# Kernel tuning notes

Measured on AMD Instinct MI355X. Metric: run time of the kernel, lower is better.

Reference implementation:

```python
import jax, jax.numpy as jnp
import numpy as np

K = 3        # kernel_size
EPS = 1e-4   # eps from __init__


def _conv_valid(x, w):
    # NHWC input, HWIO filter, VALID padding, stride 1
    return jax.lax.conv_general_dilated(
        x, w, window_strides=(1, 1), padding='VALID',
        dimension_numbers=('NHWC', 'HWIO', 'NHWC'))


def _backward_standardize_weight(grad_in, original_weights, gain, w_max_bitmap, eps):
    # Faithful translation of BackwardInjectWSConv2D.backward_standardize_weight
    kh, kw, cin, cout = original_weights.shape
    N = float(kh * kw * cin)                       # b*h*w in the TF code
    mu = jnp.mean(original_weights, axis=(0, 1, 2))
    xmu = original_weights - mu                    # [K,K,Cin,Cout]
    var = jnp.mean(jnp.square(xmu), axis=(0, 1, 2))
    mvar = N * var
    maxvar = jnp.maximum(mvar, eps)
    sqrtvar = jnp.sqrt(maxvar)
    ivar = 1.0 / sqrtvar
    givar = gain * ivar                            # [Cout]
    dgivar = jnp.sum(grad_in * xmu, axis=(0, 1, 2))
    divar = dgivar * gain
    dgain = dgivar * ivar
    dxmu1 = grad_in * givar
    dsqrtvar = (-1.0 / jnp.square(sqrtvar)) * divar
    dmaxvar = (0.5 / jnp.sqrt(maxvar)) * dsqrtvar
    dmvar = w_max_bitmap * dmaxvar
    dvar = N * dmvar
    dsq = (1.0 / N) * dvar                         # (1/N)*ones_like(grad_in)*dvar, broadcast
    dxmu2 = 2.0 * xmu * dsq
    dx1 = dxmu1 + dxmu2
    dmu = -jnp.sum(dx1, axis=(0, 1, 2))
    dx2 = (1.0 / N) * dmu                          # broadcast over [K,K,Cin]
    dx = dx1 + dx2
    return dx, dgain


def setup_inputs() -> dict:
    key = jax.random.key(0)
    ks = jax.random.split(key, 5)
    B, H, W, Cin, Cout = 64, 56, 56, 128, 128
    return {
        'grad_output': jax.random.normal(ks[0], (B, H, W, Cout), jnp.float32),
        'inputs': jax.random.normal(ks[1], (B, H, W, Cin), jnp.float32),
        'kernels': jax.random.normal(ks[2], (K, K, Cin, Cout), jnp.float32),
        'std_kernels': jax.random.normal(ks[3], (K, K, Cin, Cout), jnp.float32),
        'gain': jax.random.uniform(ks[4], (Cout,), jnp.float32),
        'w_max_bitmap': jnp.ones((Cout,), jnp.float32),
    }


def reference(grad_output, inputs, kernels, std_kernels, gain, w_max_bitmap):
    pad = (K - 1) // 2
    # ---- grad wrt input: full conv of grad_out with rot180(std_kernels), io swapped
    go_pad = jnp.pad(grad_output, ((0, 0), (pad, pad), (pad, pad), (0, 0)))
    w_rot = jnp.transpose(std_kernels[::-1, ::-1], (0, 1, 3, 2))   # [K,K,Cout,Cin]
    manual_grad_in = _conv_valid(go_pad, w_rot)                    # [B,H,W,Cin]
    # ---- grad wrt weight: treat Cin as batch, B as contraction channel
    in_pad = jnp.pad(inputs, ((0, 0), (pad, pad), (pad, pad), (0, 0)))
    fmt_inp = jnp.transpose(in_pad, (3, 1, 2, 0))                  # [Cin,H+2p,W+2p,B]
    fmt_wt = jnp.transpose(grad_output, (1, 2, 0, 3))              # [H,W,B,Cout]
    direct = _conv_valid(fmt_inp, fmt_wt)                          # [Cin,K,K,Cout]
    grad_wt_raw = jnp.transpose(direct, (1, 2, 0, 3))              # [K,K,Cin,Cout]
    # ---- weight-standardization backward chain
    manual_grad_wt, manual_grad_gain = _backward_standardize_weight(
        grad_wt_raw, kernels, gain, w_max_bitmap, EPS)
    # ---- bias grad
    manual_grad_bias = jnp.sum(grad_output, axis=(0, 1, 2))        # [Cout]
    return manual_grad_in, manual_grad_wt, manual_grad_bias, manual_grad_gain
```

## Files before the change

### kernel.cpp

```cpp
#include <hip/hip_runtime.h>
#include <hip/hip_bf16.h>

typedef __bf16 bf16x8 __attribute__((ext_vector_type(8)));
typedef __bf16 bf16x4 __attribute__((ext_vector_type(4)));
typedef float  f32x4  __attribute__((ext_vector_type(4)));
typedef unsigned int u32;

#define HW_   3136
#define NPIX  200704
#define GI_ELEMS 25690112

#define GOT_OFF   0u
#define RAW_OFF   51380224u
#define BIASA_OFF 51970048u
#define STDKF_OFF 51970560u
#define GUARD_OFF 52265472u
#define ZB_OFF    52265728u
#define ZA_OFF    52272000u
#define X_OFF     52279168u

__device__ __forceinline__ f32x4 mfma16(bf16x8 a, bf16x8 b, f32x4 c){
  return __builtin_amdgcn_mfma_f32_16x16x32_bf16(a, b, c, 0, 0, 0);
}

__device__ __forceinline__ void async16(const void* g, __bf16* l){
  __builtin_amdgcn_global_load_lds(
      (const __attribute__((address_space(1))) void*)g,
      (__attribute__((address_space(3))) void*)l, 16, 0, 0);
}

__global__ __launch_bounds__(256) void k_prep(const float* __restrict__ s, __bf16* __restrict__ d){
  const int g = blockIdx.x*256 + threadIdx.x;
  const int l = g & 63;
  const int j = (g >> 6) & 7;
  const int kc = (g >> 9) & 3;
  const int tap = g >> 11;
  const int ci = j*16 + (l & 15);
  const int co0 = kc*32 + (l >> 4)*8;
  const float* src = s + ((size_t)(tap*128 + ci))*128 + co0;
  f32x4 x0 = *(const f32x4*)src;
  f32x4 x1 = *(const f32x4*)(src + 4);
  bf16x8 y;
  #pragma unroll
  for (int e=0;e<4;e++){ y[e] = (__bf16)x0[e]; y[e+4] = (__bf16)x1[e]; }
  *(bf16x8*)(d + (size_t)g*8) = y;
}

__global__ __launch_bounds__(256) void k_goT(const float* __restrict__ go,
                                             __bf16* __restrict__ goT,
                                             __bf16* __restrict__ goB,
                                             float* __restrict__ biasA){
  __shared__ __bf16 T[64][130];
  __shared__ float biasS[128];
  const int t = threadIdx.x;
  const size_t p0 = (size_t)blockIdx.x*64;
  if (t < 128) biasS[t] = 0.f;
  __syncthreads();
  float bs[4] = {0.f,0.f,0.f,0.f};
  const int co0 = (t*4) & 127;
  #pragma unroll
  for (int i=0;i<8;i++){
    const int flat = (i*256+t)*4;
    const int px = flat >> 7, co = flat & 127;
    f32x4 x = *(const f32x4*)(go + p0*128 + flat);
    bf16x4 y;
    #pragma unroll
    for (int e=0;e<4;e++){ y[e] = (__bf16)x[e]; bs[e] += x[e]; }
    *(bf16x4*)&T[px][co] = y;
    *(bf16x4*)(goB + p0*128 + flat) = y;
  }
  #pragma unroll
  for (int e=0;e<4;e++) atomicAdd(&biasS[co0+e], bs[e]);
  __syncthreads();
  #pragma unroll
  for (int j=0;j<2;j++){
    const int task = j*256 + t;
    const int co = task >> 2, q = task & 3;
    bf16x8 v0, v1;
    #pragma unroll
    for (int k=0;k<8;k++) v0[k] = T[q*16+k][co];
    #pragma unroll
    for (int k=0;k<8;k++) v1[k] = T[q*16+8+k][co];
    __bf16* d = goT + (size_t)co*NPIX + p0 + q*16;
    *(bf16x8*)d = v0; *(bf16x8*)(d+8) = v1;
  }
  if (t < 128) atomicAdd(&biasA[t], biasS[t]);
}

__global__ __launch_bounds__(256) void k_inT(const float* __restrict__ inp,
                                             __bf16* __restrict__ inT){
  __shared__ __bf16 T[64][130];
  const int t = threadIdx.x;
  const size_t p0 = (size_t)blockIdx.x*64;

  if (blockIdx.x < 2304){
    const int g = blockIdx.x*256 + t;
    const int pair = g / 72, k = g - pair*72;
    __bf16* base = inT + (size_t)pair*3712;
    int off;
    if (k < 8)       off = k*8;
    else if (k < 16) off = 57*64 + (k-8)*8;
    else             off = (k-15)*64 + 56;
    bf16x8 z = {};
    *(bf16x8*)(base + off) = z;
  }

  #pragma unroll
  for (int i=0;i<8;i++){
    const int flat = (i*256+t)*4;
    const int px = flat >> 7, ci = flat & 127;
    f32x4 x = *(const f32x4*)(inp + p0*128 + flat);
    bf16x4 y;
    #pragma unroll
    for (int e=0;e<4;e++) y[e] = (__bf16)x[e];
    *(bf16x4*)&T[px][ci] = y;
  }
  __syncthreads();
  #pragma unroll
  for (int j=0;j<4;j++){
    const int task = j*256 + t;
    const int ci = task >> 3, ch = task & 7;
    const int p = (int)p0 + ch*8;
    const int b = p / HW_; const int r = p - b*HW_;
    const int h = r / 56;  const int w = r - h*56;
    bf16x8 v;
    #pragma unroll
    for (int k=0;k<8;k++) v[k] = T[ch*8+k][ci];
    *(bf16x8*)(inT + (((size_t)(ci*64+b))*58 + (h+1))*64 + w) = v;
  }
}

__global__ __launch_bounds__(512, 2) void k_gradin5(const __bf16* __restrict__ goB,
                                                    const __bf16* __restrict__ stdkF,
                                                    const __bf16* __restrict__ zsrc,
                                                    float* __restrict__ out){
  __shared__ char LDS[74240];
  const int t = threadIdx.x;
  const int wv = t >> 6, l = t & 63, lr = l & 15, lg = l >> 4;
  const int b = blockIdx.x, h0 = blockIdx.y*8;
  const int j0 = (wv & 1)*4;
  const int pxg = (wv >> 1)*112;

  int sb[7];
  #pragma unroll
  for (int tile=0; tile<7; ++tile){
    const int p = pxg + tile*16 + lr;
    const int ro = p / 56; const int w = p - ro*56;
    sb[tile] = (ro + 2)*58 + (w + 2);
  }

  f32x4 acc[7][4];
  #pragma unroll
  for (int i=0;i<7;i++){
    #pragma unroll
    for (int j=0;j<4;j++){
      #pragma unroll
      for (int r=0;r<4;r++) acc[i][j][r] = 0.f;
    }
  }

  for (int c=0; c<2; ++c){
    #pragma unroll
    for (int it=0; it<10; ++it){
      const int qb = it*512 + wv*64;
      const u32 q = (u32)(qb + l);
      if (q < 4640u){
        const u32 r = q / 464u;
        const u32 rem = q - r*464u;
        const u32 wp = rem >> 3;
        const u32 cl = rem & 7u;
        const int h = h0 - 1 + (int)r;
        const u32 s = r*58u + wp;
        const u32 csrc = cl ^ (s & 7u);
        const bool valid = (h >= 0) & (h < 56) & (wp >= 1u) & (wp <= 56u);
        const __bf16* src = valid
          ? goB + ((size_t)((b*HW_) + h*56 + ((int)wp - 1))*128 + c*64 + csrc*8)
          : zsrc;
        async16(src, (__bf16*)(LDS + qb*16));
      }
    }
    __syncthreads();

    for (int tap=0; tap<9; ++tap){
      const int u = tap/3;
      const int soff = u*58 + (tap - u*3);
      #pragma unroll
      for (int kc=0; kc<2; ++kc){
        const int kcg = c*2 + kc;
        bf16x8 Bf[4];
        #pragma unroll
        for (int j=0;j<4;++j)
          Bf[j] = *(const bf16x8*)(stdkF + ((size_t)(((tap*4 + kcg)*8 + j0 + j)*64 + l))*8);
        bf16x8 Af[7];
        #pragma unroll
        for (int tile=0;tile<7;++tile){
          const int s = sb[tile] - soff;
          const int byte = (s << 7) | (((kc*4 + lg) ^ (s & 7)) << 4);
          Af[tile] = *(const bf16x8*)(LDS + byte);
        }
        #pragma unroll
        for (int tile=0;tile<7;++tile){
          #pragma unroll
          for (int j=0;j<4;++j)
            acc[tile][j] = mfma16(Af[tile], Bf[j], acc[tile][j]);
        }
      }
    }
    __syncthreads();
  }

  float* o = out + ((size_t)b*HW_ + (size_t)h0*56 + pxg)*128;
  #pragma unroll
  for (int tile=0;tile<7;++tile){
    #pragma unroll
    for (int j=0;j<4;++j){
      #pragma unroll
      for (int r=0;r<4;++r)
        o[(size_t)(tile*16 + 4*lg + r)*128 + (j0 + j)*16 + lr] = acc[tile][j][r];
    }
  }
}

#define KSTEP9(ks)                                                             \
{                                                                              \
  const int pl = (ks)*32 + lg*8;                                               \
  const int q  = (ks)*4 + lg;                                                  \
  const int hl = q / 7;                                                        \
  const int w0 = pl - hl*56;                                                   \
  const int plc = ((ks)==3 && lg==3) ? 112 : pl;                               \
  bf16x8 b0 = *(const bf16x8*)&Bb[(wco + lr)*120 + plc];                       \
  bf16x8 b1 = *(const bf16x8*)&Bb[(wco + 16 + lr)*120 + plc];                  \
  const __bf16* abase = &Ab[lr*264 + hl*64 + w0];                              \
  _Pragma("unroll")                                                            \
  for (int u=0; u<3; ++u){                                                     \
    const __bf16* ap = abase + u*64;                                           \
    union { bf16x8 v; u32 d[4]; } vp, va, vn, a0, a2;                          \
    vp.v = *(const bf16x8*)(ap - 8);                                           \
    va.v = *(const bf16x8*)ap;                                                 \
    vn.v = *(const bf16x8*)(ap + 8);                                           \
    if ((ks)==3 && lg >= 2){                                                   \
      vp.d[0]=0u; vp.d[1]=0u; vp.d[2]=0u; vp.d[3]=0u;                          \
      va.d[0]=0u; va.d[1]=0u; va.d[2]=0u; va.d[3]=0u;                          \
      vn.d[0]=0u; vn.d[1]=0u; vn.d[2]=0u; vn.d[3]=0u;                          \
    }                                                                          \
    a0.d[0] = (va.d[0] << 16) | (vp.d[3] >> 16);                               \
    a0.d[1] = (va.d[1] << 16) | (va.d[0] >> 16);                               \
    a0.d[2] = (va.d[2] << 16) | (va.d[1] >> 16);                               \
    a0.d[3] = (va.d[3] << 16) | (va.d[2] >> 16);                               \
    a2.d[0] = (va.d[0] >> 16) | (va.d[1] << 16);                               \
    a2.d[1] = (va.d[1] >> 16) | (va.d[2] << 16);                               \
    a2.d[2] = (va.d[2] >> 16) | (va.d[3] << 16);                               \
    a2.d[3] = (va.d[3] >> 16) | (vn.d[0] << 16);                               \
    acc[u*3+0][0] = mfma16(a0.v, b0, acc[u*3+0][0]);                           \
    acc[u*3+0][1] = mfma16(a0.v, b1, acc[u*3+0][1]);                           \
    acc[u*3+1][0] = mfma16(va.v, b0, acc[u*3+1][0]);                           \
    acc[u*3+1][1] = mfma16(va.v, b1, acc[u*3+1][1]);                           \
    acc[u*3+2][0] = mfma16(a2.v, b0, acc[u*3+2][0]);                           \
    acc[u*3+2][1] = mfma16(a2.v, b1, acc[u*3+2][1]);                           \
  }                                                                            \
}

__global__ __launch_bounds__(256, 2) void k_gradwt9(const char* __restrict__ ws,
                                                    float* __restrict__ raw){
  __shared__ __bf16 LDS[39208];
  const int t = threadIdx.x;
  const int w = t >> 6, l = t & 63, lr = l & 15, lg = l >> 4;
  const int b = blockIdx.x, ci0 = blockIdx.y*16;
  const int wco = w*32;

  if (t < 40){
    const int idx = (t < 8) ? (30720 + t) : ((t < 24) ? (34952 + t - 8) : (39192 + t - 24));
    LDS[idx] = (__bf16)0.f;
  }

  u32 boff[8];
  #pragma unroll
  for (int i=0;i<8;i++){
    const int chunk = i*256 + t;
    if (chunk < 1920){
      const int co = chunk / 15, part = chunk - co*15;
      boff[i] = (part < 14)
        ? (GOT_OFF + (u32)(co*NPIX + b*HW_ + part*8)*2u)
        : ZB_OFF;
    } else boff[i] = ZB_OFF;
  }
  u32 aoff[3];
  #pragma unroll
  for (int i=0;i<3;i++){
    const int chunk = i*256 + t;
    if (chunk < 528){
      const int ci = chunk / 33, r = chunk - ci*33;
      aoff[i] = (r < 32)
        ? (X_OFF + (u32)((((ci0+ci)*64 + b)*58 + (r>>3))*64 + (r&7)*8)*2u)
        : ZA_OFF;
    } else aoff[i] = ZA_OFF;
  }

  f32x4 acc[9][2];
  #pragma unroll
  for (int tp=0;tp<9;tp++){
    #pragma unroll
    for (int j=0;j<2;j++){
      #pragma unroll
      for (int r=0;r<4;r++) acc[tp][j][r] = 0.f;
    }
  }

  #pragma unroll
  for (int i=0;i<8;i++){
    const int chunk = i*256 + t;
    if (chunk < 1920){ async16(ws + boff[i], LDS + chunk*8); boff[i] += 224u; }
  }
  #pragma unroll
  for (int i=0;i<3;i++){
    const int chunk = i*256 + t;
    if (chunk < 528){ async16(ws + aoff[i], LDS + 30728 + chunk*8); aoff[i] += 256u; }
  }
  __syncthreads();

  for (int c=0; c<28; ++c){
    const int cur = c & 1;
    if (c < 27){
      __bf16* dB = LDS + ((cur ^ 1) ? 15360 : 0);
      __bf16* dA = LDS + ((cur ^ 1) ? 34968 : 30728);
      #pragma unroll
      for (int i=0;i<8;i++){
        const int chunk = i*256 + t;
        if (chunk < 1920){ async16(ws + boff[i], dB + chunk*8); boff[i] += 224u; }
      }
      #pragma unroll
      for (int i=0;i<3;i++){
        const int chunk = i*256 + t;
        if (chunk < 528){ async16(ws + aoff[i], dA + chunk*8); aoff[i] += 256u; }
      }
    }
    const __bf16* Bb = LDS + (cur ? 15360 : 0);
    const __bf16* Ab = LDS + (cur ? 34968 : 30728);
    KSTEP9(0) KSTEP9(1) KSTEP9(2) KSTEP9(3)
    __syncthreads();
  }

  #pragma unroll
  for (int tp=0;tp<9;tp++){
    #pragma unroll
    for (int j=0;j<2;j++){
      #pragma unroll
      for (int r=0;r<4;r++)
        atomicAdd(&raw[(size_t)(tp*128 + ci0 + 4*lg + r)*128 + wco + j*16 + lr],
                  acc[tp][j][r]);
    }
  }
}

__global__ __launch_bounds__(128) void k_std(const float* __restrict__ raw,
      const float* __restrict__ kern, const float* __restrict__ gain,
      const float* __restrict__ bmap, const float* __restrict__ biasA,
      float* __restrict__ out_wt, float* __restrict__ out_bias, float* __restrict__ out_gain){
  const int co = blockIdx.x, t = threadIdx.x;
  float kv[9], gv[9];
  float s1=0.f, s2=0.f, sg=0.f, sgk=0.f;
  #pragma unroll
  for (int i=0;i<9;i++){
    const int m = t + i*128;
    const float k_ = kern[(size_t)m*128 + co];
    const float g_ = raw [(size_t)m*128 + co];
    kv[i]=k_; gv[i]=g_;
    s1 += k_; s2 += k_*k_; sg += g_; sgk += g_*k_;
  }
  __shared__ float red[4][128];
  red[0][t]=s1; red[1][t]=s2; red[2][t]=sg; red[3][t]=sgk;
  __syncthreads();
  for (int off=64; off>0; off>>=1){
    if (t < off){
      red[0][t]+=red[0][t+off]; red[1][t]+=red[1][t+off];
      red[2][t]+=red[2][t+off]; red[3][t]+=red[3][t+off];
    }
    __syncthreads();
  }
  const float N = 1152.f;
  const float S1=red[0][0], S2=red[1][0], Sg=red[2][0], Sgk=red[3][0];
  const float mu = S1/N;
  const float var = S2/N - mu*mu;
  const float mvar = N*var;
  const float maxvar = fmaxf(mvar, 1e-4f);
  const float sqrtvar = sqrtf(maxvar);
  const float ivar = 1.f/sqrtvar;
  const float g = gain[co];
  const float givar = g*ivar;
  const float dgivar = Sgk - mu*Sg;
  const float divar = dgivar*g;
  const float dsqrtvar = -divar/maxvar;
  const float dmaxvar = 0.5f*dsqrtvar/sqrtvar;
  const float dsq = bmap[co]*dmaxvar;
  const float dmu = -(givar*Sg + 2.f*dsq*(S1 - N*mu));
  const float dmuN = dmu*(1.f/N);
  #pragma unroll
  for (int i=0;i<9;i++){
    const int m = t + i*128;
    out_wt[(size_t)m*128 + co] = gv[i]*givar + 2.f*(kv[i]-mu)*dsq + dmuN;
  }
  if (t == 0){ out_gain[co] = dgivar*ivar; out_bias[co] = biasA[co]; }
}

extern "C" void kernel_launch(void* const* d_in, const int* in_sizes, int n_in,
                              void* d_out, int out_size, void* d_ws, size_t ws_size,
                              hipStream_t stream){
  const float* go   = (const float*)d_in[0];
  const float* inp  = (const float*)d_in[1];
  const float* kern = (const float*)d_in[2];
  const float* stdk = (const float*)d_in[3];
  const float* gain = (const float*)d_in[4];
  const float* bmap = (const float*)d_in[5];

  char* ws = (char*)d_ws;
  __bf16* goT   = (__bf16*)(ws + GOT_OFF);
  float*  raw   = (float*) (ws + RAW_OFF);
  float*  biasA = (float*) (ws + BIASA_OFF);
  __bf16* stdkF = (__bf16*)(ws + STDKF_OFF);
  char*   guard =           ws + GUARD_OFF;
  __bf16* goB   = (__bf16*)(ws + X_OFF);
  __bf16* inT   = (__bf16*)(ws + X_OFF);

  hipMemsetAsync(ws + RAW_OFF,   0, 589824 + 512, stream);
  hipMemsetAsync(ws + GUARD_OFF, 0, 256 + 6272 + 7168, stream);

  k_prep  <<<72, 256, 0, stream>>>(stdk, stdkF);
  k_goT   <<<3136, 256, 0, stream>>>(go, goT, goB, biasA);
  k_gradin5<<<dim3(64,7), 512, 0, stream>>>(goB, stdkF, (const __bf16*)guard, (float*)d_out);

  k_inT   <<<3136, 256, 0, stream>>>(inp, inT);
  k_gradwt9<<<dim3(64,8), 256, 0, stream>>>((const char*)ws, raw);

  float* out = (float*)d_out;
  k_std<<<128, 128, 0, stream>>>(raw, kern, gain, bmap, biasA,
                                 out + GI_ELEMS,
                                 out + GI_ELEMS + 147456,
                                 out + GI_ELEMS + 147456 + 128);
}
```

Before: 300.5 us.

## Split weight-gradient kernel over image halves and drop double buffering for occupancy

The weight-gradient kernel now splits each image's rows into two halves via a third grid dimension, which doubles the block count and adds more atomic accumulation into the raw buffer. The double-buffered LDS pipeline is replaced by a single buffer with load, sync, compute, sync. This halves shared memory per block so the launch bound can allow four blocks per CU instead of two. The aim is to hide memory latency through occupancy and more parallel blocks rather than software prefetch, at the cost of exposed load latency within each block and twice the atomics.

```diff
diff --git a/kernel.cpp b/kernel.cpp
--- a/kernel.cpp
+++ b/kernel.cpp
@@ -221,16 +221,20 @@
   }
 }
 
-#define KSTEP9(ks)                                                             \
+#define GWX_G0 15360
+#define GWX_A  15368
+#define GWX_G1 19592
+
+#define KSTEP10(ks)                                                            \
 {                                                                              \
   const int pl = (ks)*32 + lg*8;                                               \
   const int q  = (ks)*4 + lg;                                                  \
   const int hl = q / 7;                                                        \
   const int w0 = pl - hl*56;                                                   \
   const int plc = ((ks)==3 && lg==3) ? 112 : pl;                               \
-  bf16x8 b0 = *(const bf16x8*)&Bb[(wco + lr)*120 + plc];                       \
-  bf16x8 b1 = *(const bf16x8*)&Bb[(wco + 16 + lr)*120 + plc];                  \
-  const __bf16* abase = &Ab[lr*264 + hl*64 + w0];                              \
+  bf16x8 b0 = *(const bf16x8*)&LDS[(wco + lr)*120 + plc];                      \
+  bf16x8 b1 = *(const bf16x8*)&LDS[(wco + 16 + lr)*120 + plc];                 \
+  const __bf16* abase = &LDS[GWX_A + lr*264 + hl*64 + w0];                     \
   _Pragma("unroll")                                                            \
   for (int u=0; u<3; ++u){                                                     \
     const __bf16* ap = abase + u*64;                                           \
@@ -260,19 +264,20 @@
   }                                                                            \
 }
 
-__global__ __launch_bounds__(256, 2) void k_gradwt9(const char* __restrict__ ws,
-                                                    float* __restrict__ raw){
-  __shared__ __bf16 LDS[39208];
+__global__ __launch_bounds__(256, 4) void k_gradwt10(const char* __restrict__ ws,
+                                                     float* __restrict__ raw){
+  __shared__ __bf16 LDS[19608];
   const int t = threadIdx.x;
   const int w = t >> 6, l = t & 63, lr = l & 15, lg = l >> 4;
-  const int b = blockIdx.x, ci0 = blockIdx.y*16;
+  const int b = blockIdx.x, ci0 = blockIdx.y*16, hh = blockIdx.z;
   const int wco = w*32;
 
-  if (t < 40){
-    const int idx = (t < 8) ? (30720 + t) : ((t < 24) ? (34952 + t - 8) : (39192 + t - 24));
+  if (t < 24){
+    const int idx = (t < 8) ? (GWX_G0 + t) : (GWX_G1 + t - 8);
     LDS[idx] = (__bf16)0.f;
   }
 
+  const int pixbase = b*HW_ + hh*1568;
   u32 boff[8];
   #pragma unroll
   for (int i=0;i<8;i++){
@@ -280,7 +285,7 @@
     if (chunk < 1920){
       const int co = chunk / 15, part = chunk - co*15;
       boff[i] = (part < 14)
-        ? (GOT_OFF + (u32)(co*NPIX + b*HW_ + part*8)*2u)
+        ? (GOT_OFF + (u32)(co*NPIX + pixbase + part*8)*2u)
         : ZB_OFF;
     } else boff[i] = ZB_OFF;
   }
@@ -291,7 +296,7 @@
     if (chunk < 528){
       const int ci = chunk / 33, r = chunk - ci*33;
       aoff[i] = (r < 32)
-        ? (X_OFF + (u32)((((ci0+ci)*64 + b)*58 + (r>>3))*64 + (r&7)*8)*2u)
+        ? (X_OFF + (u32)((((ci0+ci)*64 + b)*58 + (r>>3) + 28*hh)*64 + (r&7)*8)*2u)
         : ZA_OFF;
     } else aoff[i] = ZA_OFF;
   }
@@ -306,37 +311,21 @@
     }
   }
 
-  #pragma unroll
-  for (int i=0;i<8;i++){
-    const int chunk = i*256 + t;
-    if (chunk < 1920){ async16(ws + boff[i], LDS + chunk*8); boff[i] += 224u; }
-  }
-  #pragma unroll
-  for (int i=0;i<3;i++){
-    const int chunk = i*256 + t;
-    if (chunk < 528){ async16(ws + aoff[i], LDS + 30728 + chunk*8); aoff[i] += 256u; }
-  }
-  __syncthreads();
-
-  for (int c=0; c<28; ++c){
-    const int cur = c & 1;
-    if (c < 27){
-      __bf16* dB = LDS + ((cur ^ 1) ? 15360 : 0);
-      __bf16* dA = LDS + ((cur ^ 1) ? 34968 : 30728);
-      #pragma unroll
-      for (int i=0;i<8;i++){
-        const int chunk = i*256 + t;
-        if (chunk < 1920){ async16(ws + boff[i], dB + chunk*8); boff[i] += 224u; }
-      }
-      #pragma unroll
-      for (int i=0;i<3;i++){
-        const int chunk = i*256 + t;
-        if (chunk < 528){ async16(ws + aoff[i], dA + chunk*8); aoff[i] += 256u; }
-      }
-    }
-    const __bf16* Bb = LDS + (cur ? 15360 : 0);
-    const __bf16* Ab = LDS + (cur ? 34968 : 30728);
-    KSTEP9(0) KSTEP9(1) KSTEP9(2) KSTEP9(3)
+  for (int c=0; c<14; ++c){
+    #pragma unroll
+    for (int i=0;i<8;i++){
+      const int chunk = i*256 + t;
+      if (chunk < 1920){ async16(ws + boff[i], LDS + chunk*8); boff[i] += 224u; }
+    }
+    #pragma unroll
+    for (int i=0;i<3;i++){
+      const int chunk = i*256 + t;
+      if (chunk < 528){ async16(ws + aoff[i], LDS + GWX_A + chunk*8); aoff[i] += 256u; }
+    }
+    __syncthreads();
+
+    KSTEP10(0) KSTEP10(1) KSTEP10(2) KSTEP10(3)
+
     __syncthreads();
   }
 
@@ -429,7 +418,7 @@
   k_gradin5<<<dim3(64,7), 512, 0, stream>>>(goB, stdkF, (const __bf16*)guard, (float*)d_out);
 
   k_inT   <<<3136, 256, 0, stream>>>(inp, inT);
-  k_gradwt9<<<dim3(64,8), 256, 0, stream>>>((const char*)ws, raw);
+  k_gradwt10<<<dim3(64,8,2), 256, 0, stream>>>((const char*)ws, raw);
 
   float* out = (float*)d_out;
   k_std<<<128, 128, 0, stream>>>(raw, kern, gain, bmap, biasA,
```

Result: slower. 414.3 us (+37.9%).
